# Kernel tuning notes

Hardware: AMD Instinct MI355X
Metric: run time of the kernel (lower is better)

The kernel has to match this reference:

```python
import jax, jax.numpy as jnp
import numpy as np

B, S, D, H = 2, 2048, 1024, 16
DK = D // H

def setup_inputs() -> dict:
    key = jax.random.key(0)
    ks = jax.random.split(key, 12)
    s = 1.0 / np.sqrt(D)
    return {
        "q": jax.random.normal(ks[0], (B, S, D), jnp.float32),
        "k": jax.random.normal(ks[1], (B, S, D), jnp.float32),
        "v": jax.random.normal(ks[2], (B, S, D), jnp.float32),
        "mask": jnp.ones((1, 1, S, S), jnp.int32),
        "Wq": jax.random.normal(ks[3], (D, D), jnp.float32) * s,
        "bq": jnp.zeros((D,), jnp.float32),
        "Wk": jax.random.normal(ks[4], (D, D), jnp.float32) * s,
        "bk": jnp.zeros((D,), jnp.float32),
        "Wv": jax.random.normal(ks[5], (D, D), jnp.float32) * s,
        "bv": jnp.zeros((D,), jnp.float32),
        "Wo": jax.random.normal(ks[6], (D, D), jnp.float32) * s,
        "bo": jnp.zeros((D,), jnp.float32),
    }

def reference(q, k, v, mask, Wq, bq, Wk, bk, Wv, bv, Wo, bo):
    # projections (torch Linear: x @ W^T + b)
    Q = q @ Wq.T + bq
    K = k @ Wk.T + bk
    V = v @ Wv.T + bv
    # split heads: [B,S,D] -> [B,H,S,DK]
    def split(x):
        return x.reshape(B, S, H, DK).transpose(0, 2, 1, 3)
    Qh, Kh, Vh = split(Q), split(K), split(V)
    scores = jnp.einsum('bhqd,bhkd->bhqk', Qh, Kh) / jnp.sqrt(jnp.float32(DK))
    scores = jnp.where(mask == 0, jnp.float32(-1e9), scores)
    attn = jax.nn.softmax(scores, axis=-1)  # dropout p=0.0 -> identity
    x = jnp.einsum('bhqk,bhkd->bhqd', attn, Vh)
    x = x.transpose(0, 2, 1, 3).reshape(B, S, D)
    return x @ Wo.T + bo
```

## Files before the change

kernel.cpp:

```cpp
#include <hip/hip_runtime.h>
#include <hip/hip_bf16.h>
#include <stdint.h>

#define B_    2
#define S_    2048
#define D_    1024
#define H_    16
#define NTOK  (B_ * S_)

typedef __attribute__((ext_vector_type(8))) short bf16x8;
typedef __attribute__((ext_vector_type(4))) float f32x4;

static __device__ __forceinline__ unsigned short f2bf(float f) {
    unsigned int u = __float_as_uint(f);
    unsigned int r = (u + 0x7FFFu + ((u >> 16) & 1u)) >> 16;
    return (unsigned short)r;
}

using g_cu32 = __attribute__((address_space(1))) const unsigned int;
using l_u32  = __attribute__((address_space(3))) unsigned int;
static __device__ __forceinline__ void gld16(const void* g, void* l) {
    __builtin_amdgcn_global_load_lds((g_cu32*)g, (l_u32*)l, 16, 0, 0);
}

#define QN ((size_t)NTOK * D_)
#define WN ((size_t)D_ * D_)

__global__ __launch_bounds__(256) void convert_kernel(
    const float* __restrict__ q, const float* __restrict__ k, const float* __restrict__ v,
    const float* __restrict__ Wq, const float* __restrict__ Wk,
    const float* __restrict__ Wv, const float* __restrict__ Wo,
    unsigned short* __restrict__ qb, unsigned short* __restrict__ kb,
    unsigned short* __restrict__ vb, unsigned short* __restrict__ wqb,
    unsigned short* __restrict__ wkb, unsigned short* __restrict__ wvb,
    unsigned short* __restrict__ wob) {
    size_t i = ((size_t)blockIdx.x * 256 + threadIdx.x) * 8;
    const float* s; unsigned short* d; size_t off;
    if (i < QN)          { s = q; d = qb; off = i; }
    else if (i < 2 * QN) { s = k; d = kb; off = i - QN; }
    else if (i < 3 * QN) { s = v; d = vb; off = i - 2 * QN; }
    else {
        size_t j = i - 3 * QN;
        int wi = (int)(j >> 20);
        s = (wi == 0) ? Wq : (wi == 1) ? Wk : (wi == 2) ? Wv : Wo;
        d = (wi == 0) ? wqb : (wi == 1) ? wkb : (wi == 2) ? wvb : wob;
        off = j & (WN - 1);
    }
    float4 a = *(const float4*)(s + off);
    float4 b = *(const float4*)(s + off + 4);
    ushort4 lo, hi;
    lo.x = f2bf(a.x); lo.y = f2bf(a.y); lo.z = f2bf(a.z); lo.w = f2bf(a.w);
    hi.x = f2bf(b.x); hi.y = f2bf(b.y); hi.z = f2bf(b.z); hi.w = f2bf(b.w);
    *(ushort4*)(d + off) = lo;
    *(ushort4*)(d + off + 4) = hi;
}

__global__ __launch_bounds__(256) void mask_flags_kernel(
    const int* __restrict__ mask, int* __restrict__ flags) {
    __shared__ int anyz;
    if (threadIdx.x == 0) anyz = 0;
    __syncthreads();
    const int qt = blockIdx.x, kt = blockIdx.y;
    int az = 0;
    for (int i = threadIdx.x; i < 64 * 64; i += 256) {
        int r = i >> 6, c = i & 63;
        az |= (mask[(size_t)(qt * 64 + r) * S_ + kt * 64 + c] == 0) ? 1 : 0;
    }
    if (az) atomicOr(&anyz, 1);
    __syncthreads();
    if (threadIdx.x == 0) flags[qt * (S_ / 64) + kt] = anyz;
}

struct GemmArgs {
    const unsigned short* A[3];
    const unsigned short* W[3];
    const float* bias[3];
    void* C[3];
    int mode[3];
};

__global__ __launch_bounds__(256, 3) void gemm_async(GemmArgs ga) {
    const int z = blockIdx.z;
    const unsigned short* __restrict__ A = ga.A[z];
    const unsigned short* __restrict__ W = ga.W[z];
    const float* __restrict__ bias = ga.bias[z];
    void* C = ga.C[z];
    const int mode = ga.mode[z];

    __shared__ unsigned short As[8 * 512];
    __shared__ unsigned short Bs[8 * 512];

    const int t    = threadIdx.x;
    const int lane = t & 63;
    const int w    = t >> 6;
    const int fr   = lane & 15;
    const int kq   = lane >> 4;
    const int wrow = w >> 1, wcol = w & 1;
    const int m0 = blockIdx.x * 128, n0 = blockIdx.y * 128;

    const int sc = lane >> 4;
    const int sr = lane & 15;
    const unsigned short* ga0 = A + (size_t)(m0 + (2 * w) * 16 + sr) * D_ + sc * 8;
    const unsigned short* ga1 = ga0 + 16 * D_;
    const unsigned short* gw0 = W + (size_t)(n0 + (2 * w) * 16 + sr) * D_ + sc * 8;
    const unsigned short* gw1 = gw0 + 16 * D_;
    unsigned short* la0 = &As[(2 * w) * 512];
    unsigned short* la1 = &As[(2 * w + 1) * 512];
    unsigned short* lw0 = &Bs[(2 * w) * 512];
    unsigned short* lw1 = &Bs[(2 * w + 1) * 512];

    int aOff[4], bOff[4];
#pragma unroll
    for (int mi = 0; mi < 4; ++mi) aOff[mi] = (wrow * 4 + mi) * 512 + (kq * 16 + fr) * 8;
#pragma unroll
    for (int ni = 0; ni < 4; ++ni) bOff[ni] = (wcol * 4 + ni) * 512 + (kq * 16 + fr) * 8;

    f32x4 acc[4][4];
#pragma unroll
    for (int i = 0; i < 4; ++i)
#pragma unroll
        for (int j = 0; j < 4; ++j) acc[i][j] = (f32x4)0.0f;

    for (int k0 = 0; k0 < D_ / 32; ++k0) {
        gld16(ga0, la0);
        gld16(ga1, la1);
        gld16(gw0, lw0);
        gld16(gw1, lw1);
        ga0 += 32; ga1 += 32; gw0 += 32; gw1 += 32;
        __syncthreads();

        bf16x8 af[4], bfr[4];
#pragma unroll
        for (int mi = 0; mi < 4; ++mi) af[mi] = *(const bf16x8*)&As[aOff[mi]];
#pragma unroll
        for (int ni = 0; ni < 4; ++ni) bfr[ni] = *(const bf16x8*)&Bs[bOff[ni]];
#pragma unroll
        for (int mi = 0; mi < 4; ++mi)
#pragma unroll
            for (int ni = 0; ni < 4; ++ni)
                acc[mi][ni] = __builtin_amdgcn_mfma_f32_16x16x32_bf16(
                    af[mi], bfr[ni], acc[mi][ni], 0, 0, 0);
        __syncthreads();
    }

    if (mode == 0) {
        float* Co = (float*)C;
#pragma unroll
        for (int ni = 0; ni < 4; ++ni) {
            int col = n0 + wcol * 64 + ni * 16 + fr;
            float bv = bias[col];
#pragma unroll
            for (int mi = 0; mi < 4; ++mi)
#pragma unroll
                for (int r = 0; r < 4; ++r) {
                    int row = m0 + wrow * 64 + mi * 16 + kq * 4 + r;
                    Co[(size_t)row * D_ + col] = acc[mi][ni][r] + bv;
                }
        }
    } else if (mode == 1) {
        unsigned short* Co = (unsigned short*)C;
#pragma unroll
        for (int ni = 0; ni < 4; ++ni) {
            int col = n0 + wcol * 64 + ni * 16 + fr;
            float bv = bias[col];
#pragma unroll
            for (int mi = 0; mi < 4; ++mi)
#pragma unroll
                for (int r = 0; r < 4; ++r) {
                    int row = m0 + wrow * 64 + mi * 16 + kq * 4 + r;
                    Co[(size_t)row * D_ + col] = f2bf(acc[mi][ni][r] + bv);
                }
        }
    } else {
        unsigned short* Co = (unsigned short*)C;
#pragma unroll
        for (int ni = 0; ni < 4; ++ni) {
            int col = n0 + wcol * 64 + ni * 16 + fr;
            float bv = bias[col];
            int hh = col >> 6, d = col & 63;
#pragma unroll
            for (int mi = 0; mi < 4; ++mi) {
                int tok = m0 + wrow * 64 + mi * 16 + kq * 4;
                int bb = tok >> 11, sbase = tok & (S_ - 1);
                ushort4 pk;
                pk.x = f2bf(acc[mi][ni][0] + bv);
                pk.y = f2bf(acc[mi][ni][1] + bv);
                pk.z = f2bf(acc[mi][ni][2] + bv);
                pk.w = f2bf(acc[mi][ni][3] + bv);
                *(ushort4*)(Co + ((size_t)((bb * H_ + hh) * 64 + d)) * S_ + sbase) = pk;
            }
        }
    }
}

__global__ __launch_bounds__(512, 4) void flash2(
    const unsigned short* __restrict__ Qb, const unsigned short* __restrict__ Kb,
    const unsigned short* __restrict__ Vtg, const int* __restrict__ mask,
    const int* __restrict__ flags, unsigned short* __restrict__ Xb) {
    __shared__ unsigned short PQ[8 * 16 * 72];
    __shared__ unsigned short Ks[4 * 1024];
    __shared__ unsigned short Vs[4 * 1024];

    const int t    = threadIdx.x;
    const int lane = t & 63;
    const int w    = t >> 6;
    const int fr   = lane & 15;
    const int kq   = lane >> 4;
    const int qt = blockIdx.x, hd = blockIdx.y, b = blockIdx.z;
    const int q0 = qt * 128;

    {
        const int rr = lane & 15, c4 = lane >> 4;
#pragma unroll
        for (int j = 0; j < 2; ++j) {
            int i = w * 2 + j, g = i >> 1, half = i & 1;
            gld16(Qb + (size_t)(b * S_ + q0 + g * 16 + rr) * D_ + hd * 64 + (half * 4 + c4) * 8,
                  (char*)PQ + i * 1024);
        }
    }
    __syncthreads();

    bf16x8 qf[2];
#pragma unroll
    for (int kk = 0; kk < 2; ++kk)
        qf[kk] = *(const bf16x8*)&PQ[w * 1024 + ((kk * 4 + kq) * 16 + fr) * 8];

    f32x4 o[4];
#pragma unroll
    for (int i = 0; i < 4; ++i) o[i] = (f32x4)0.0f;
    float m_i = -INFINITY, l_i = 0.0f;

    const float SC = 0.18033688011112042f;
    const int frow = (q0 + w * 16) >> 6;

    const int srow = lane & 15, schunk = lane >> 4;
    const unsigned short* kbase =
        Kb + (size_t)(b * S_ + ((w >> 1) * 16) + srow) * D_ + hd * 64 + ((w & 1) * 4 + schunk) * 8;
    const unsigned short* vbase =
        Vtg + ((size_t)((b * H_ + hd) * 64 + (w >> 1) * 16 + srow)) * S_ + ((w & 1) * 4 + schunk) * 8;

    for (int kt = 0; kt < S_ / 64; ++kt) {
        __syncthreads();
        gld16(kbase + (size_t)kt * 64 * D_, (char*)Ks + w * 1024);
        gld16(vbase + (size_t)kt * 64, (char*)Vs + w * 1024);
        __syncthreads();

        f32x4 st[4];
#pragma unroll
        for (int mi = 0; mi < 4; ++mi) st[mi] = (f32x4)0.0f;
#pragma unroll
        for (int kk = 0; kk < 2; ++kk)
#pragma unroll
            for (int mi = 0; mi < 4; ++mi) {
                bf16x8 a = *(const bf16x8*)&Ks[mi * 1024 + ((kk * 4 + kq) * 16 + fr) * 8];
                st[mi] = __builtin_amdgcn_mfma_f32_16x16x32_bf16(a, qf[kk], st[mi], 0, 0, 0);
            }

        float p[4][4];
#pragma unroll
        for (int mi = 0; mi < 4; ++mi)
#pragma unroll
            for (int r = 0; r < 4; ++r) p[mi][r] = st[mi][r] * SC;

        if (flags[frow * (S_ / 64) + kt]) {
#pragma unroll
            for (int mi = 0; mi < 4; ++mi) {
                int4 mv = *(const int4*)&mask[(size_t)(q0 + w * 16 + fr) * S_ + kt * 64 + mi * 16 + kq * 4];
                if (mv.x == 0) p[mi][0] = -3e8f;
                if (mv.y == 0) p[mi][1] = -3e8f;
                if (mv.z == 0) p[mi][2] = -3e8f;
                if (mv.w == 0) p[mi][3] = -3e8f;
            }
        }

        float mx = -INFINITY;
#pragma unroll
        for (int mi = 0; mi < 4; ++mi)
            mx = fmaxf(mx, fmaxf(fmaxf(p[mi][0], p[mi][1]), fmaxf(p[mi][2], p[mi][3])));
        mx = fmaxf(mx, __shfl_xor(mx, 16, 64));
        mx = fmaxf(mx, __shfl_xor(mx, 32, 64));
        float mn = fmaxf(m_i, mx);
        float alpha = exp2f(m_i - mn);
        m_i = mn;
        float ps = 0.0f;
#pragma unroll
        for (int mi = 0; mi < 4; ++mi)
#pragma unroll
            for (int r = 0; r < 4; ++r) {
                p[mi][r] = exp2f(p[mi][r] - mn);
                ps += p[mi][r];
            }
        ps += __shfl_xor(ps, 16, 64);
        ps += __shfl_xor(ps, 32, 64);
        l_i = l_i * alpha + ps;

#pragma unroll
        for (int mi = 0; mi < 4; ++mi) {
            ushort4 pk;
            pk.x = f2bf(p[mi][0]); pk.y = f2bf(p[mi][1]);
            pk.z = f2bf(p[mi][2]); pk.w = f2bf(p[mi][3]);
            *(ushort4*)&PQ[w * 1152 + fr * 72 + mi * 16 + kq * 4] = pk;
        }
#pragma unroll
        for (int mi = 0; mi < 4; ++mi)
#pragma unroll
            for (int r = 0; r < 4; ++r) o[mi][r] *= alpha;

#pragma unroll
        for (int kk = 0; kk < 2; ++kk) {
            bf16x8 pb = *(const bf16x8*)&PQ[w * 1152 + fr * 72 + kk * 32 + kq * 8];
#pragma unroll
            for (int mi = 0; mi < 4; ++mi) {
                bf16x8 a = *(const bf16x8*)&Vs[mi * 1024 + ((kk * 4 + kq) * 16 + fr) * 8];
                o[mi] = __builtin_amdgcn_mfma_f32_16x16x32_bf16(a, pb, o[mi], 0, 0, 0);
            }
        }
    }

    float rl = 1.0f / l_i;
#pragma unroll
    for (int mi = 0; mi < 4; ++mi) {
        ushort4 pk;
        pk.x = f2bf(o[mi][0] * rl); pk.y = f2bf(o[mi][1] * rl);
        pk.z = f2bf(o[mi][2] * rl); pk.w = f2bf(o[mi][3] * rl);
        *(ushort4*)(Xb + (size_t)(b * S_ + q0 + w * 16 + fr) * D_ + hd * 64 + mi * 16 + kq * 4) = pk;
    }
}

extern "C" void kernel_launch(void* const* d_in, const int* in_sizes, int n_in,
                              void* d_out, int out_size, void* d_ws, size_t ws_size,
                              hipStream_t stream) {
    const float* q    = (const float*)d_in[0];
    const float* k    = (const float*)d_in[1];
    const float* v    = (const float*)d_in[2];
    const int*   mask = (const int*)d_in[3];
    const float* Wq   = (const float*)d_in[4];
    const float* bq   = (const float*)d_in[5];
    const float* Wk   = (const float*)d_in[6];
    const float* bk   = (const float*)d_in[7];
    const float* Wv   = (const float*)d_in[8];
    const float* bv   = (const float*)d_in[9];
    const float* Wo   = (const float*)d_in[10];
    const float* bo   = (const float*)d_in[11];
    float* out = (float*)d_out;

    unsigned short* qb  = (unsigned short*)d_ws;
    unsigned short* kb  = qb + QN;
    unsigned short* vb  = kb + QN;
    unsigned short* Qf  = vb + QN;
    unsigned short* Kf  = Qf + QN;
    unsigned short* Vt  = Kf + QN;
    unsigned short* wqb = Vt + QN;
    unsigned short* wkb = wqb + WN;
    unsigned short* wvb = wkb + WN;
    unsigned short* wob = wvb + WN;
    int* flags = (int*)(wob + WN);

    convert_kernel<<<8192, 256, 0, stream>>>(q, k, v, Wq, Wk, Wv, Wo,
                                             qb, kb, vb, wqb, wkb, wvb, wob);
    mask_flags_kernel<<<dim3(S_ / 64, S_ / 64), 256, 0, stream>>>(mask, flags);

    GemmArgs g1;
    g1.A[0] = qb;  g1.W[0] = wqb; g1.bias[0] = bq; g1.C[0] = Qf; g1.mode[0] = 1;
    g1.A[1] = kb;  g1.W[1] = wkb; g1.bias[1] = bk; g1.C[1] = Kf; g1.mode[1] = 1;
    g1.A[2] = vb;  g1.W[2] = wvb; g1.bias[2] = bv; g1.C[2] = Vt; g1.mode[2] = 2;
    gemm_async<<<dim3(NTOK / 128, D_ / 128, 3), 256, 0, stream>>>(g1);

    flash2<<<dim3(S_ / 128, H_, B_), 512, 0, stream>>>(Qf, Kf, Vt, mask, flags, Qf);

    GemmArgs g2;
    g2.A[0] = Qf; g2.W[0] = wob; g2.bias[0] = bo; g2.C[0] = out; g2.mode[0] = 0;
    g2.A[1] = g2.A[2] = nullptr; g2.W[1] = g2.W[2] = nullptr;
    g2.bias[1] = g2.bias[2] = nullptr; g2.C[1] = g2.C[2] = nullptr;
    g2.mode[1] = g2.mode[2] = 0;
    gemm_async<<<dim3(NTOK / 128, D_ / 128, 1), 256, 0, stream>>>(g2);
}
```

Baseline: 312.5 us.

## Shrink attention tiles, fold softmax scale into Q projection, packed bf16 converts

The flash kernel moves from 128-query blocks with 8 waves to 64-query blocks with 4 waves, which doubles the grid. Mask flags are preloaded once per block via a ballot instead of a global load per tile, and the O rescale is skipped when no lane's max changed. The softmax scale is folded into the Q projection epilogue. The output GEMM uses 64-row tiles for more blocks, and bf16 conversion uses packed hardware converts. Smaller attention tiles reload K/V more often relative to the compute done on them.

```diff
diff --git a/kernel.cpp b/kernel.cpp
--- a/kernel.cpp
+++ b/kernel.cpp
@@ -10,11 +10,20 @@
 
 typedef __attribute__((ext_vector_type(8))) short bf16x8;
 typedef __attribute__((ext_vector_type(4))) float f32x4;
+typedef __attribute__((ext_vector_type(2))) float float2v;
+typedef __attribute__((ext_vector_type(2))) __bf16 bfv2;
 
 static __device__ __forceinline__ unsigned short f2bf(float f) {
     unsigned int u = __float_as_uint(f);
     unsigned int r = (u + 0x7FFFu + ((u >> 16) & 1u)) >> 16;
     return (unsigned short)r;
+}
+static __device__ __forceinline__ unsigned int pkbf(float a, float b) {
+    float2v fv = {a, b};
+    bfv2 r = __builtin_convertvector(fv, bfv2);
+    unsigned int u;
+    __builtin_memcpy(&u, &r, 4);
+    return u;
 }
 
 using g_cu32 = __attribute__((address_space(1))) const unsigned int;
@@ -48,11 +57,10 @@
     }
     float4 a = *(const float4*)(s + off);
     float4 b = *(const float4*)(s + off + 4);
-    ushort4 lo, hi;
-    lo.x = f2bf(a.x); lo.y = f2bf(a.y); lo.z = f2bf(a.z); lo.w = f2bf(a.w);
-    hi.x = f2bf(b.x); hi.y = f2bf(b.y); hi.z = f2bf(b.z); hi.w = f2bf(b.w);
-    *(ushort4*)(d + off) = lo;
-    *(ushort4*)(d + off + 4) = hi;
+    uint4 pk;
+    pk.x = pkbf(a.x, a.y); pk.y = pkbf(a.z, a.w);
+    pk.z = pkbf(b.x, b.y); pk.w = pkbf(b.z, b.w);
+    *(uint4*)(d + off) = pk;
 }
 
 __global__ __launch_bounds__(256) void mask_flags_kernel(
@@ -77,17 +85,22 @@
     const float* bias[3];
     void* C[3];
     int mode[3];
+    float scale[3];
 };
 
+template<int BMT>
 __global__ __launch_bounds__(256, 3) void gemm_async(GemmArgs ga) {
+    constexpr int AG = BMT / 16;
+    constexpr int MI = BMT / 32;
     const int z = blockIdx.z;
     const unsigned short* __restrict__ A = ga.A[z];
     const unsigned short* __restrict__ W = ga.W[z];
     const float* __restrict__ bias = ga.bias[z];
     void* C = ga.C[z];
     const int mode = ga.mode[z];
-
-    __shared__ unsigned short As[8 * 512];
+    const float scl = ga.scale[z];
+
+    __shared__ unsigned short As[AG * 512];
     __shared__ unsigned short Bs[8 * 512];
 
     const int t    = threadIdx.x;
@@ -96,46 +109,57 @@
     const int fr   = lane & 15;
     const int kq   = lane >> 4;
     const int wrow = w >> 1, wcol = w & 1;
-    const int m0 = blockIdx.x * 128, n0 = blockIdx.y * 128;
+    const int m0 = blockIdx.x * BMT, n0 = blockIdx.y * 128;
 
     const int sc = lane >> 4;
     const int sr = lane & 15;
-    const unsigned short* ga0 = A + (size_t)(m0 + (2 * w) * 16 + sr) * D_ + sc * 8;
-    const unsigned short* ga1 = ga0 + 16 * D_;
+
+    const unsigned short* ga0;
+    const unsigned short* ga1 = nullptr;
+    unsigned short* la0;
+    unsigned short* la1 = nullptr;
+    if constexpr (BMT == 128) {
+        ga0 = A + (size_t)(m0 + (2 * w) * 16 + sr) * D_ + sc * 8;
+        ga1 = ga0 + 16 * D_;
+        la0 = &As[(2 * w) * 512];
+        la1 = &As[(2 * w + 1) * 512];
+    } else {
+        ga0 = A + (size_t)(m0 + w * 16 + sr) * D_ + sc * 8;
+        la0 = &As[w * 512];
+    }
     const unsigned short* gw0 = W + (size_t)(n0 + (2 * w) * 16 + sr) * D_ + sc * 8;
     const unsigned short* gw1 = gw0 + 16 * D_;
-    unsigned short* la0 = &As[(2 * w) * 512];
-    unsigned short* la1 = &As[(2 * w + 1) * 512];
     unsigned short* lw0 = &Bs[(2 * w) * 512];
     unsigned short* lw1 = &Bs[(2 * w + 1) * 512];
 
-    int aOff[4], bOff[4];
-#pragma unroll
-    for (int mi = 0; mi < 4; ++mi) aOff[mi] = (wrow * 4 + mi) * 512 + (kq * 16 + fr) * 8;
+    int aOff[MI], bOff[4];
+#pragma unroll
+    for (int mi = 0; mi < MI; ++mi) aOff[mi] = (wrow * MI + mi) * 512 + (kq * 16 + fr) * 8;
 #pragma unroll
     for (int ni = 0; ni < 4; ++ni) bOff[ni] = (wcol * 4 + ni) * 512 + (kq * 16 + fr) * 8;
 
-    f32x4 acc[4][4];
-#pragma unroll
-    for (int i = 0; i < 4; ++i)
+    f32x4 acc[MI][4];
+#pragma unroll
+    for (int i = 0; i < MI; ++i)
 #pragma unroll
         for (int j = 0; j < 4; ++j) acc[i][j] = (f32x4)0.0f;
 
     for (int k0 = 0; k0 < D_ / 32; ++k0) {
         gld16(ga0, la0);
-        gld16(ga1, la1);
+        if constexpr (BMT == 128) gld16(ga1, la1);
         gld16(gw0, lw0);
         gld16(gw1, lw1);
-        ga0 += 32; ga1 += 32; gw0 += 32; gw1 += 32;
+        ga0 += 32; gw0 += 32; gw1 += 32;
+        if constexpr (BMT == 128) ga1 += 32;
         __syncthreads();
 
-        bf16x8 af[4], bfr[4];
-#pragma unroll
-        for (int mi = 0; mi < 4; ++mi) af[mi] = *(const bf16x8*)&As[aOff[mi]];
+        bf16x8 af[MI], bfr[4];
+#pragma unroll
+        for (int mi = 0; mi < MI; ++mi) af[mi] = *(const bf16x8*)&As[aOff[mi]];
 #pragma unroll
         for (int ni = 0; ni < 4; ++ni) bfr[ni] = *(const bf16x8*)&Bs[bOff[ni]];
 #pragma unroll
-        for (int mi = 0; mi < 4; ++mi)
+        for (int mi = 0; mi < MI; ++mi)
 #pragma unroll
             for (int ni = 0; ni < 4; ++ni)
                 acc[mi][ni] = __builtin_amdgcn_mfma_f32_16x16x32_bf16(
@@ -150,11 +174,11 @@
             int col = n0 + wcol * 64 + ni * 16 + fr;
             float bv = bias[col];
 #pragma unroll
-            for (int mi = 0; mi < 4; ++mi)
+            for (int mi = 0; mi < MI; ++mi)
 #pragma unroll
                 for (int r = 0; r < 4; ++r) {
-                    int row = m0 + wrow * 64 + mi * 16 + kq * 4 + r;
-                    Co[(size_t)row * D_ + col] = acc[mi][ni][r] + bv;
+                    int row = m0 + wrow * (BMT / 2) + mi * 16 + kq * 4 + r;
+                    Co[(size_t)row * D_ + col] = (acc[mi][ni][r] + bv) * scl;
                 }
         }
     } else if (mode == 1) {
@@ -164,11 +188,11 @@
             int col = n0 + wcol * 64 + ni * 16 + fr;
             float bv = bias[col];
 #pragma unroll
-            for (int mi = 0; mi < 4; ++mi)
+            for (int mi = 0; mi < MI; ++mi)
 #pragma unroll
                 for (int r = 0; r < 4; ++r) {
-                    int row = m0 + wrow * 64 + mi * 16 + kq * 4 + r;
-                    Co[(size_t)row * D_ + col] = f2bf(acc[mi][ni][r] + bv);
+                    int row = m0 + wrow * (BMT / 2) + mi * 16 + kq * 4 + r;
+                    Co[(size_t)row * D_ + col] = f2bf((acc[mi][ni][r] + bv) * scl);
                 }
         }
     } else {
@@ -179,27 +203,25 @@
             float bv = bias[col];
             int hh = col >> 6, d = col & 63;
 #pragma unroll
-            for (int mi = 0; mi < 4; ++mi) {
-                int tok = m0 + wrow * 64 + mi * 16 + kq * 4;
+            for (int mi = 0; mi < MI; ++mi) {
+                int tok = m0 + wrow * (BMT / 2) + mi * 16 + kq * 4;
                 int bb = tok >> 11, sbase = tok & (S_ - 1);
-                ushort4 pk;
-                pk.x = f2bf(acc[mi][ni][0] + bv);
-                pk.y = f2bf(acc[mi][ni][1] + bv);
-                pk.z = f2bf(acc[mi][ni][2] + bv);
-                pk.w = f2bf(acc[mi][ni][3] + bv);
-                *(ushort4*)(Co + ((size_t)((bb * H_ + hh) * 64 + d)) * S_ + sbase) = pk;
+                uint2 pk;
+                pk.x = pkbf((acc[mi][ni][0] + bv) * scl, (acc[mi][ni][1] + bv) * scl);
+                pk.y = pkbf((acc[mi][ni][2] + bv) * scl, (acc[mi][ni][3] + bv) * scl);
+                *(uint2*)(Co + ((size_t)((bb * H_ + hh) * 64 + d)) * S_ + sbase) = pk;
             }
         }
     }
 }
 
-__global__ __launch_bounds__(512, 4) void flash2(
+__global__ __launch_bounds__(256, 4) void flash3(
     const unsigned short* __restrict__ Qb, const unsigned short* __restrict__ Kb,
     const unsigned short* __restrict__ Vtg, const int* __restrict__ mask,
     const int* __restrict__ flags, unsigned short* __restrict__ Xb) {
-    __shared__ unsigned short PQ[8 * 16 * 72];
-    __shared__ unsigned short Ks[4 * 1024];
-    __shared__ unsigned short Vs[4 * 1024];
+    __shared__ unsigned short PQ[4608];
+    __shared__ unsigned short Ks[4096];
+    __shared__ unsigned short Vs[4096];
 
     const int t    = threadIdx.x;
     const int lane = t & 63;
@@ -207,17 +229,17 @@
     const int fr   = lane & 15;
     const int kq   = lane >> 4;
     const int qt = blockIdx.x, hd = blockIdx.y, b = blockIdx.z;
-    const int q0 = qt * 128;
-
-    {
-        const int rr = lane & 15, c4 = lane >> 4;
-#pragma unroll
-        for (int j = 0; j < 2; ++j) {
-            int i = w * 2 + j, g = i >> 1, half = i & 1;
-            gld16(Qb + (size_t)(b * S_ + q0 + g * 16 + rr) * D_ + hd * 64 + (half * 4 + c4) * 8,
-                  (char*)PQ + i * 1024);
-        }
-    }
+    const int q0 = qt * 64;
+
+    const int rr = lane & 15, c4 = lane >> 4;
+#pragma unroll
+    for (int j = 0; j < 2; ++j)
+        gld16(Qb + (size_t)(b * S_ + q0 + w * 16 + rr) * D_ + hd * 64 + (j * 4 + c4) * 8,
+              (char*)PQ + w * 2048 + j * 1024);
+
+    int fl = (lane < 32) ? flags[qt * 32 + lane] : 0;
+    unsigned int fmask = (unsigned int)__ballot(fl != 0);
+
     __syncthreads();
 
     bf16x8 qf[2];
@@ -230,19 +252,18 @@
     for (int i = 0; i < 4; ++i) o[i] = (f32x4)0.0f;
     float m_i = -INFINITY, l_i = 0.0f;
 
-    const float SC = 0.18033688011112042f;
-    const int frow = (q0 + w * 16) >> 6;
-
-    const int srow = lane & 15, schunk = lane >> 4;
     const unsigned short* kbase =
-        Kb + (size_t)(b * S_ + ((w >> 1) * 16) + srow) * D_ + hd * 64 + ((w & 1) * 4 + schunk) * 8;
+        Kb + (size_t)(b * S_ + w * 16 + rr) * D_ + hd * 64 + (c4)*8;
     const unsigned short* vbase =
-        Vtg + ((size_t)((b * H_ + hd) * 64 + (w >> 1) * 16 + srow)) * S_ + ((w & 1) * 4 + schunk) * 8;
+        Vtg + ((size_t)((b * H_ + hd) * 64 + w * 16 + rr)) * S_ + (c4)*8;
 
     for (int kt = 0; kt < S_ / 64; ++kt) {
         __syncthreads();
-        gld16(kbase + (size_t)kt * 64 * D_, (char*)Ks + w * 1024);
-        gld16(vbase + (size_t)kt * 64, (char*)Vs + w * 1024);
+#pragma unroll
+        for (int j = 0; j < 2; ++j) {
+            gld16(kbase + (size_t)kt * 64 * D_ + j * 32, (char*)Ks + w * 2048 + j * 1024);
+            gld16(vbase + (size_t)kt * 64 + j * 32, (char*)Vs + w * 2048 + j * 1024);
+        }
         __syncthreads();
 
         f32x4 st[4];
@@ -260,9 +281,9 @@
 #pragma unroll
         for (int mi = 0; mi < 4; ++mi)
 #pragma unroll
-            for (int r = 0; r < 4; ++r) p[mi][r] = st[mi][r] * SC;
-
-        if (flags[frow * (S_ / 64) + kt]) {
+            for (int r = 0; r < 4; ++r) p[mi][r] = st[mi][r];
+
+        if ((fmask >> kt) & 1u) {
 #pragma unroll
             for (int mi = 0; mi < 4; ++mi) {
                 int4 mv = *(const int4*)&mask[(size_t)(q0 + w * 16 + fr) * S_ + kt * 64 + mi * 16 + kq * 4];
@@ -296,15 +317,18 @@
 
 #pragma unroll
         for (int mi = 0; mi < 4; ++mi) {
-            ushort4 pk;
-            pk.x = f2bf(p[mi][0]); pk.y = f2bf(p[mi][1]);
-            pk.z = f2bf(p[mi][2]); pk.w = f2bf(p[mi][3]);
-            *(ushort4*)&PQ[w * 1152 + fr * 72 + mi * 16 + kq * 4] = pk;
-        }
-#pragma unroll
-        for (int mi = 0; mi < 4; ++mi)
-#pragma unroll
-            for (int r = 0; r < 4; ++r) o[mi][r] *= alpha;
+            uint2 pk;
+            pk.x = pkbf(p[mi][0], p[mi][1]);
+            pk.y = pkbf(p[mi][2], p[mi][3]);
+            *(uint2*)&PQ[w * 1152 + fr * 72 + mi * 16 + kq * 4] = pk;
+        }
+
+        if (__ballot(alpha != 1.0f)) {
+#pragma unroll
+            for (int mi = 0; mi < 4; ++mi)
+#pragma unroll
+                for (int r = 0; r < 4; ++r) o[mi][r] *= alpha;
+        }
 
 #pragma unroll
         for (int kk = 0; kk < 2; ++kk) {
@@ -320,10 +344,10 @@
     float rl = 1.0f / l_i;
 #pragma unroll
     for (int mi = 0; mi < 4; ++mi) {
-        ushort4 pk;
-        pk.x = f2bf(o[mi][0] * rl); pk.y = f2bf(o[mi][1] * rl);
-        pk.z = f2bf(o[mi][2] * rl); pk.w = f2bf(o[mi][3] * rl);
-        *(ushort4*)(Xb + (size_t)(b * S_ + q0 + w * 16 + fr) * D_ + hd * 64 + mi * 16 + kq * 4) = pk;
+        uint2 pk;
+        pk.x = pkbf(o[mi][0] * rl, o[mi][1] * rl);
+        pk.y = pkbf(o[mi][2] * rl, o[mi][3] * rl);
+        *(uint2*)(Xb + (size_t)(b * S_ + q0 + w * 16 + fr) * D_ + hd * 64 + mi * 16 + kq * 4) = pk;
     }
 }
 
@@ -356,22 +380,24 @@
     unsigned short* wob = wvb + WN;
     int* flags = (int*)(wob + WN);
 
+    const float SC = 0.18033688011112042f;
+
     convert_kernel<<<8192, 256, 0, stream>>>(q, k, v, Wq, Wk, Wv, Wo,
                                              qb, kb, vb, wqb, wkb, wvb, wob);
     mask_flags_kernel<<<dim3(S_ / 64, S_ / 64), 256, 0, stream>>>(mask, flags);
 
     GemmArgs g1;
-    g1.A[0] = qb;  g1.W[0] = wqb; g1.bias[0] = bq; g1.C[0] = Qf; g1.mode[0] = 1;
-    g1.A[1] = kb;  g1.W[1] = wkb; g1.bias[1] = bk; g1.C[1] = Kf; g1.mode[1] = 1;
-    g1.A[2] = vb;  g1.W[2] = wvb; g1.bias[2] = bv; g1.C[2] = Vt; g1.mode[2] = 2;
-    gemm_async<<<dim3(NTOK / 128, D_ / 128, 3), 256, 0, stream>>>(g1);
-
-    flash2<<<dim3(S_ / 128, H_, B_), 512, 0, stream>>>(Qf, Kf, Vt, mask, flags, Qf);
+    g1.A[0] = qb;  g1.W[0] = wqb; g1.bias[0] = bq; g1.C[0] = Qf; g1.mode[0] = 1; g1.scale[0] = SC;
+    g1.A[1] = kb;  g1.W[1] = wkb; g1.bias[1] = bk; g1.C[1] = Kf; g1.mode[1] = 1; g1.scale[1] = 1.0f;
+    g1.A[2] = vb;  g1.W[2] = wvb; g1.bias[2] = bv; g1.C[2] = Vt; g1.mode[2] = 2; g1.scale[2] = 1.0f;
+    gemm_async<128><<<dim3(NTOK / 128, D_ / 128, 3), 256, 0, stream>>>(g1);
+
+    flash3<<<dim3(S_ / 64, H_, B_), 256, 0, stream>>>(Qf, Kf, Vt, mask, flags, Qf);
 
     GemmArgs g2;
-    g2.A[0] = Qf; g2.W[0] = wob; g2.bias[0] = bo; g2.C[0] = out; g2.mode[0] = 0;
+    g2.A[0] = Qf; g2.W[0] = wob; g2.bias[0] = bo; g2.C[0] = out; g2.mode[0] = 0; g2.scale[0] = 1.0f;
     g2.A[1] = g2.A[2] = nullptr; g2.W[1] = g2.W[2] = nullptr;
     g2.bias[1] = g2.bias[2] = nullptr; g2.C[1] = g2.C[2] = nullptr;
-    g2.mode[1] = g2.mode[2] = 0;
-    gemm_async<<<dim3(NTOK / 128, D_ / 128, 1), 256, 0, stream>>>(g2);
-}
+    g2.mode[1] = g2.mode[2] = 0; g2.scale[1] = g2.scale[2] = 1.0f;
+    gemm_async<64><<<dim3(NTOK / 64, D_ / 128, 1), 256, 0, stream>>>(g2);
+}
```

Result: faster. 297.7 us (-4.7%).
